# Optimization experiments

Measured on AMD Instinct MI355X. Metric: run time of the kernel, lower is better.

The kernel has to match this reference:

```python
import jax, jax.numpy as jnp
import numpy as np

NUM_HEADS = 16
HEAD_DIM = 64  # hidden_size // num_heads


def _logsparse_allowed(seq_len):
    # allowed[i, j] True if key j is attended by query i:
    # j == i, j == i-1, or j == i - 2^k (k >= 1); combined with causal (j <= i).
    i = jnp.arange(seq_len)[:, None]
    j = jnp.arange(seq_len)[None, :]
    diff = i - j
    pow2 = (diff > 0) & ((diff & (diff - 1)) == 0)  # covers diff==1 and diff==2^k
    return (diff == 0) | pow2  # implies diff >= 0, so causal is subsumed


def setup_inputs() -> dict:
    key = jax.random.key(0)
    ks = jax.random.split(key, 7)
    B, S, H = 4, 2048, 1024
    return {
        "hidden_states": jax.random.normal(ks[0], (B, S, H), dtype=jnp.float32),
        "attention_mask": jnp.zeros((B, 1, 1, S), dtype=jnp.float32),
        "Wq": jax.random.normal(ks[1], (H, H), dtype=jnp.float32) * 0.02,
        "bq": jnp.zeros((H,), dtype=jnp.float32),
        "Wk": jax.random.normal(ks[2], (H, H), dtype=jnp.float32) * 0.02,
        "bk": jnp.zeros((H,), dtype=jnp.float32),
        "Wv": jax.random.normal(ks[3], (H, H), dtype=jnp.float32) * 0.02,
        "bv": jnp.zeros((H,), dtype=jnp.float32),
    }


def _split_heads(x):
    B, S, _ = x.shape
    return x.reshape(B, S, NUM_HEADS, HEAD_DIM).transpose(0, 2, 1, 3)  # b h t d


def reference(hidden_states, attention_mask, Wq, bq, Wk, bk, Wv, bv):
    B, S, H = hidden_states.shape
    q = _split_heads(hidden_states @ Wq.T + bq)
    k = _split_heads(hidden_states @ Wk.T + bk)
    v = _split_heads(hidden_states @ Wv.T + bv)

    scores = jnp.einsum("bhqd,bhkd->bhqk", q, k) * (HEAD_DIM ** -0.5)
    allowed = _logsparse_allowed(S)  # [S, S] bool
    scores = jnp.where(allowed[None, None], scores, -jnp.inf)
    scores = scores + attention_mask  # [B,1,1,S] additive mask
    probs = jax.nn.softmax(scores, axis=-1)
    out = jnp.einsum("bhqk,bhkd->bhqd", probs, v)
    return out.transpose(0, 2, 1, 3).reshape(B, S, H)
```

## Files before the change

### kernel.cpp

```cpp
#include <hip/hip_runtime.h>
#include <hip/hip_bf16.h>

#define S_LEN   2048
#define NHEADS  16
#define HDIM    64
#define HID     1024
#define BATCH   4
#define M_ROWS  (BATCH * S_LEN)

#define BM 128
#define BN 128
#define BK 64

typedef __attribute__((ext_vector_type(8))) short short8;
typedef __attribute__((ext_vector_type(4))) float floatx4;
typedef __attribute__((ext_vector_type(16))) float floatx16;
typedef __attribute__((ext_vector_type(4))) unsigned short ushort4v;

__device__ __forceinline__ unsigned short f2bf_rne(float x) {
  union { float f; unsigned u; } v; v.f = x;
  unsigned r = v.u + 0x7fffu + ((v.u >> 16) & 1u);
  return (unsigned short)(r >> 16);
}

__device__ __forceinline__ float bf2f(unsigned short u) {
  union { unsigned u; float f; } c; c.u = ((unsigned)u) << 16;
  return c.f;
}

__device__ __forceinline__ void glds16(const unsigned short* g, unsigned short* l) {
  __builtin_amdgcn_global_load_lds(
      (const __attribute__((address_space(1))) unsigned int*)g,
      (__attribute__((address_space(3))) unsigned int*)l, 16, 0, 0);
}

#define HS4 (M_ROWS * HID / 4)
#define W4  (HID * HID / 4)
__global__ __launch_bounds__(256) void cast_all(
    const float* __restrict__ hs, const float* __restrict__ Wq,
    const float* __restrict__ Wk, const float* __restrict__ Wv,
    unsigned short* __restrict__ hsb, unsigned short* __restrict__ wqb,
    unsigned short* __restrict__ wkb, unsigned short* __restrict__ wvb) {
  int idx = blockIdx.x * 256 + threadIdx.x;
  const float* in;
  unsigned short* out;
  int off;
  if (idx < HS4) {
    in = hs; out = hsb; off = idx;
  } else {
    int r = idx - HS4;
    int seg = r >> 18;
    off = r & (W4 - 1);
    in  = (seg == 0) ? Wq  : (seg == 1) ? Wk  : Wv;
    out = (seg == 0) ? wqb : (seg == 1) ? wkb : wvb;
  }
  floatx4 v = __builtin_nontemporal_load((const floatx4*)in + off);
  ushort4v o;
  o.x = f2bf_rne(v.x);
  o.y = f2bf_rne(v.y);
  o.z = f2bf_rne(v.z);
  o.w = f2bf_rne(v.w);
  ((ushort4v*)out)[off] = o;
}

__global__ __launch_bounds__(256) void qkv_gemm(
    const unsigned short* __restrict__ A,
    const unsigned short* __restrict__ W0, const unsigned short* __restrict__ W1,
    const unsigned short* __restrict__ W2,
    const float* __restrict__ b0, const float* __restrict__ b1,
    const float* __restrict__ b2,
    unsigned short* __restrict__ O0, unsigned short* __restrict__ O1,
    unsigned short* __restrict__ O2) {
  const int K = HID;
  const int N = HID;
  const int z = blockIdx.z;
  const unsigned short* __restrict__ W = (z == 0) ? W0 : (z == 1) ? W1 : W2;
  const float* __restrict__ bias = (z == 0) ? b0 : (z == 1) ? b1 : b2;
  unsigned short* __restrict__ O = (z == 0) ? O0 : (z == 1) ? O1 : O2;

  __shared__ __align__(16) unsigned short As[BM * BK];
  __shared__ __align__(16) unsigned short Bs[BN * BK];

  const int tid = threadIdx.x;
  const int w = tid >> 6;
  const int lane = tid & 63;
  const int m0 = blockIdx.x * BM;
  const int n0 = blockIdx.y * BN;

  const int lr = lane >> 3;
  const int cc = (lane & 7) ^ lr;
  const unsigned short* gA[4];
  const unsigned short* gB[4];
  unsigned short* lA[4];
  unsigned short* lB[4];
  #pragma unroll
  for (int u = 0; u < 4; ++u) {
    const int seg = w * 4 + u;
    const int r = seg * 8 + lr;
    gA[u] = A + (size_t)(m0 + r) * K + cc * 8;
    gB[u] = W + (size_t)(n0 + r) * K + cc * 8;
    lA[u] = As + seg * 512;
    lB[u] = Bs + seg * 512;
  }

  const int lrow32 = lane & 31;
  const int kgrp = lane >> 5;
  const int sw = lane & 7;
  const int arow = (w & 1) * 64;
  const int brow = (w >> 1) * 64;

  floatx16 acc[2][2] = {};

  for (int k0 = 0; k0 < K; k0 += BK) {
    #pragma unroll
    for (int u = 0; u < 4; ++u) {
      glds16(gA[u] + k0, lA[u]);
      glds16(gB[u] + k0, lB[u]);
    }
    __syncthreads();

    #pragma unroll
    for (int s = 0; s < 4; ++s) {
      const int cp = (((s << 1) | kgrp) ^ sw) * 8;
      short8 af[2], bf[2];
      #pragma unroll
      for (int im = 0; im < 2; ++im)
        af[im] = *(const short8*)(As + (arow + im * 32 + lrow32) * BK + cp);
      #pragma unroll
      for (int in = 0; in < 2; ++in)
        bf[in] = *(const short8*)(Bs + (brow + in * 32 + lrow32) * BK + cp);

      #pragma unroll
      for (int im = 0; im < 2; ++im)
        #pragma unroll
        for (int in = 0; in < 2; ++in)
          acc[im][in] = __builtin_amdgcn_mfma_f32_32x32x16_bf16(af[im], bf[in], acc[im][in], 0, 0, 0);
    }
    __syncthreads();
  }

  #pragma unroll
  for (int im = 0; im < 2; ++im) {
    #pragma unroll
    for (int in = 0; in < 2; ++in) {
      const int col = n0 + brow + in * 32 + lrow32;
      const float bb = bias[col];
      const int rowbase = m0 + arow + im * 32 + 4 * kgrp;
      #pragma unroll
      for (int reg = 0; reg < 16; ++reg) {
        const int row = rowbase + (reg & 3) + 8 * (reg >> 2);
        O[(size_t)row * N + col] = f2bf_rne(acc[im][in][reg] + bb);
      }
    }
  }
}

__global__ __launch_bounds__(256) void logsparse_attn(
    const unsigned short* __restrict__ Q, const unsigned short* __restrict__ K,
    const unsigned short* __restrict__ V, const float* __restrict__ mask,
    float* __restrict__ out) {
  const int bid = (blockIdx.x & 7) * 512 + (blockIdx.x >> 3);
  const int tid = threadIdx.x;
  const int l = tid & 7;
  const int qglob = bid * 32 + (tid >> 3);

  const int i = qglob & (S_LEN - 1);
  const int h = (qglob >> 11) & (NHEADS - 1);
  const int b = qglob >> 15;

  const size_t base = (size_t)b * S_LEN * HID + h * HDIM + l * 8;

  int js[12];
  js[0] = i;
  int nj = 1;
  for (int d = 1; d <= i; d <<= 1) js[nj++] = i - d;
  #pragma unroll
  for (int t = 0; t < 12; ++t)
    if (t >= nj) js[t] = i;

  short8 k8[12];
  #pragma unroll
  for (int t = 0; t < 12; ++t)
    k8[t] = *(const short8*)(K + base + (size_t)js[t] * HID);
  const short8 q8 = *(const short8*)(Q + base + (size_t)i * HID);
  float mk[12];
  #pragma unroll
  for (int t = 0; t < 12; ++t)
    mk[t] = mask[b * S_LEN + js[t]];

  float qf[8];
  #pragma unroll
  for (int e = 0; e < 8; ++e) qf[e] = bf2f((unsigned short)q8[e]);

  float s[12];
  #pragma unroll
  for (int t = 0; t < 12; ++t) {
    float p = 0.f;
    #pragma unroll
    for (int e = 0; e < 8; ++e) p += qf[e] * bf2f((unsigned short)k8[t][e]);
    p += __shfl_xor(p, 1, 64);
    p += __shfl_xor(p, 2, 64);
    p += __shfl_xor(p, 4, 64);
    s[t] = (t < nj) ? (p * 0.125f + mk[t]) : -1e30f;
  }

  float mx = s[0];
  #pragma unroll
  for (int t = 1; t < 12; ++t) mx = fmaxf(mx, s[t]);
  float lsum = 0.f;
  #pragma unroll
  for (int t = 0; t < 12; ++t) { s[t] = __expf(s[t] - mx); lsum += s[t]; }
  const float inv = 1.f / lsum;

  short8 v8[12];
  #pragma unroll
  for (int t = 0; t < 12; ++t)
    v8[t] = *(const short8*)(V + base + (size_t)js[t] * HID);

  float o[8] = {};
  #pragma unroll
  for (int t = 0; t < 12; ++t) {
    #pragma unroll
    for (int e = 0; e < 8; ++e) o[e] += s[t] * bf2f((unsigned short)v8[t][e]);
  }

  float* op = out + base + (size_t)i * HID;
  floatx4 o0 = {o[0] * inv, o[1] * inv, o[2] * inv, o[3] * inv};
  floatx4 o1 = {o[4] * inv, o[5] * inv, o[6] * inv, o[7] * inv};
  __builtin_nontemporal_store(o0, (floatx4*)op);
  __builtin_nontemporal_store(o1, (floatx4*)(op + 4));
}

extern "C" void kernel_launch(void* const* d_in, const int* in_sizes, int n_in,
                              void* d_out, int out_size, void* d_ws, size_t ws_size,
                              hipStream_t stream) {
  const float* hs   = (const float*)d_in[0];
  const float* mask = (const float*)d_in[1];
  const float* Wq   = (const float*)d_in[2];
  const float* bq   = (const float*)d_in[3];
  const float* Wk   = (const float*)d_in[4];
  const float* bk   = (const float*)d_in[5];
  const float* Wv   = (const float*)d_in[6];
  const float* bv   = (const float*)d_in[7];
  float* out = (float*)d_out;

  unsigned short* hsb = (unsigned short*)d_ws;
  unsigned short* wqb = hsb + (size_t)M_ROWS * HID;
  unsigned short* wkb = wqb + (size_t)HID * HID;
  unsigned short* wvb = wkb + (size_t)HID * HID;
  unsigned short* Qb = wvb + (size_t)HID * HID;
  unsigned short* Kb = Qb + (size_t)M_ROWS * HID;
  unsigned short* Vb = Kb + (size_t)M_ROWS * HID;

  {
    int quads = HS4 + 3 * W4;
    cast_all<<<quads / 256, 256, 0, stream>>>(hs, Wq, Wk, Wv, hsb, wqb, wkb, wvb);
  }

  {
    dim3 grid(M_ROWS / BM, HID / BN, 3);
    qkv_gemm<<<grid, 256, 0, stream>>>(hsb, wqb, wkb, wvb, bq, bk, bv, Qb, Kb, Vb);
  }

  {
    int blocks = (BATCH * NHEADS * S_LEN) / 32;
    logsparse_attn<<<blocks, 256, 0, stream>>>(Qb, Kb, Vb, mask, out);
  }
}
```

Measured before the change: 181.1 us.

## Interleave K and V per head and retune GEMM LDS swizzle

The QKV GEMM now writes K and V into one interleaved buffer: each head's 64 K columns sit next to its 64 V columns in each 128-element row segment. The attention kernel uses 16 lanes per query, split into two halves that load K and V from the same row at once. The halves exchange dot products with a shuffle, and only the V half writes output. The LDS swizzle also XORs in the segment index to change the bank mapping. This aims to make the gathered K/V rows contiguous 256-byte reads and to cut per-thread register use, at the cost of twice as many threads and redundant softmax work in each half.

```diff
diff --git a/kernel.cpp b/kernel.cpp
--- a/kernel.cpp
+++ b/kernel.cpp
@@ -69,14 +69,11 @@
     const unsigned short* __restrict__ W2,
     const float* __restrict__ b0, const float* __restrict__ b1,
     const float* __restrict__ b2,
-    unsigned short* __restrict__ O0, unsigned short* __restrict__ O1,
-    unsigned short* __restrict__ O2) {
+    unsigned short* __restrict__ Qo, unsigned short* __restrict__ KVo) {
   const int K = HID;
-  const int N = HID;
   const int z = blockIdx.z;
   const unsigned short* __restrict__ W = (z == 0) ? W0 : (z == 1) ? W1 : W2;
   const float* __restrict__ bias = (z == 0) ? b0 : (z == 1) ? b1 : b2;
-  unsigned short* __restrict__ O = (z == 0) ? O0 : (z == 1) ? O1 : O2;
 
   __shared__ __align__(16) unsigned short As[BM * BK];
   __shared__ __align__(16) unsigned short Bs[BN * BK];
@@ -88,7 +85,6 @@
   const int n0 = blockIdx.y * BN;
 
   const int lr = lane >> 3;
-  const int cc = (lane & 7) ^ lr;
   const unsigned short* gA[4];
   const unsigned short* gB[4];
   unsigned short* lA[4];
@@ -96,6 +92,7 @@
   #pragma unroll
   for (int u = 0; u < 4; ++u) {
     const int seg = w * 4 + u;
+    const int cc = (lane & 7) ^ lr ^ (2 * (seg & 3));
     const int r = seg * 8 + lr;
     gA[u] = A + (size_t)(m0 + r) * K + cc * 8;
     gB[u] = W + (size_t)(n0 + r) * K + cc * 8;
@@ -105,7 +102,7 @@
 
   const int lrow32 = lane & 31;
   const int kgrp = lane >> 5;
-  const int sw = lane & 7;
+  const int sw = (lane & 7) ^ (2 * ((lane >> 3) & 3));
   const int arow = (w & 1) * 64;
   const int brow = (w >> 1) * 64;
 
@@ -139,36 +136,42 @@
     __syncthreads();
   }
 
+  unsigned short* const Ob = (z == 0) ? Qo : KVo;
+  const int ostride = (z == 0) ? HID : 2 * HID;
   #pragma unroll
   for (int im = 0; im < 2; ++im) {
     #pragma unroll
     for (int in = 0; in < 2; ++in) {
       const int col = n0 + brow + in * 32 + lrow32;
       const float bb = bias[col];
+      const int ocol = (z == 0) ? col
+                                : ((col >> 6) * 128 + (col & 63) + ((z == 2) ? 64 : 0));
       const int rowbase = m0 + arow + im * 32 + 4 * kgrp;
       #pragma unroll
       for (int reg = 0; reg < 16; ++reg) {
         const int row = rowbase + (reg & 3) + 8 * (reg >> 2);
-        O[(size_t)row * N + col] = f2bf_rne(acc[im][in][reg] + bb);
+        Ob[(size_t)row * ostride + ocol] = f2bf_rne(acc[im][in][reg] + bb);
       }
     }
   }
 }
 
 __global__ __launch_bounds__(256) void logsparse_attn(
-    const unsigned short* __restrict__ Q, const unsigned short* __restrict__ K,
-    const unsigned short* __restrict__ V, const float* __restrict__ mask,
-    float* __restrict__ out) {
-  const int bid = (blockIdx.x & 7) * 512 + (blockIdx.x >> 3);
+    const unsigned short* __restrict__ Q, const unsigned short* __restrict__ KV,
+    const float* __restrict__ mask, float* __restrict__ out) {
+  const int bid = (blockIdx.x & 7) * 1024 + (blockIdx.x >> 3);
   const int tid = threadIdx.x;
-  const int l = tid & 7;
-  const int qglob = bid * 32 + (tid >> 3);
+  const int l = tid & 15;
+  const int half = l >> 3;
+  const int e8 = (l & 7) * 8;
+  const int qglob = bid * 16 + (tid >> 4);
 
   const int i = qglob & (S_LEN - 1);
   const int h = (qglob >> 11) & (NHEADS - 1);
   const int b = qglob >> 15;
 
-  const size_t base = (size_t)b * S_LEN * HID + h * HDIM + l * 8;
+  const size_t qaddr  = ((size_t)b * S_LEN + i) * HID + h * HDIM + e8;
+  const size_t kvbase = (size_t)b * S_LEN * (2 * HID) + h * 128 + half * 64 + e8;
 
   int js[12];
   js[0] = i;
@@ -178,11 +181,11 @@
   for (int t = 0; t < 12; ++t)
     if (t >= nj) js[t] = i;
 
-  short8 k8[12];
+  short8 kv[12];
   #pragma unroll
   for (int t = 0; t < 12; ++t)
-    k8[t] = *(const short8*)(K + base + (size_t)js[t] * HID);
-  const short8 q8 = *(const short8*)(Q + base + (size_t)i * HID);
+    kv[t] = *(const short8*)(KV + kvbase + (size_t)js[t] * (2 * HID));
+  const short8 q8 = *(const short8*)(Q + qaddr);
   float mk[12];
   #pragma unroll
   for (int t = 0; t < 12; ++t)
@@ -197,11 +200,13 @@
   for (int t = 0; t < 12; ++t) {
     float p = 0.f;
     #pragma unroll
-    for (int e = 0; e < 8; ++e) p += qf[e] * bf2f((unsigned short)k8[t][e]);
+    for (int e = 0; e < 8; ++e) p += qf[e] * bf2f((unsigned short)kv[t][e]);
     p += __shfl_xor(p, 1, 64);
     p += __shfl_xor(p, 2, 64);
     p += __shfl_xor(p, 4, 64);
-    s[t] = (t < nj) ? (p * 0.125f + mk[t]) : -1e30f;
+    const float px = __shfl_xor(p, 8, 64);
+    const float sc = half ? px : p;
+    s[t] = (t < nj) ? (sc * 0.125f + mk[t]) : -1e30f;
   }
 
   float mx = s[0];
@@ -212,23 +217,20 @@
   for (int t = 0; t < 12; ++t) { s[t] = __expf(s[t] - mx); lsum += s[t]; }
   const float inv = 1.f / lsum;
 
-  short8 v8[12];
-  #pragma unroll
-  for (int t = 0; t < 12; ++t)
-    v8[t] = *(const short8*)(V + base + (size_t)js[t] * HID);
-
   float o[8] = {};
   #pragma unroll
   for (int t = 0; t < 12; ++t) {
     #pragma unroll
-    for (int e = 0; e < 8; ++e) o[e] += s[t] * bf2f((unsigned short)v8[t][e]);
-  }
-
-  float* op = out + base + (size_t)i * HID;
-  floatx4 o0 = {o[0] * inv, o[1] * inv, o[2] * inv, o[3] * inv};
-  floatx4 o1 = {o[4] * inv, o[5] * inv, o[6] * inv, o[7] * inv};
-  __builtin_nontemporal_store(o0, (floatx4*)op);
-  __builtin_nontemporal_store(o1, (floatx4*)(op + 4));
+    for (int e = 0; e < 8; ++e) o[e] += s[t] * bf2f((unsigned short)kv[t][e]);
+  }
+
+  if (half) {
+    float* op = out + ((size_t)b * S_LEN + i) * HID + h * HDIM + e8;
+    floatx4 o0 = {o[0] * inv, o[1] * inv, o[2] * inv, o[3] * inv};
+    floatx4 o1 = {o[4] * inv, o[5] * inv, o[6] * inv, o[7] * inv};
+    __builtin_nontemporal_store(o0, (floatx4*)op);
+    __builtin_nontemporal_store(o1, (floatx4*)(op + 4));
+  }
 }
 
 extern "C" void kernel_launch(void* const* d_in, const int* in_sizes, int n_in,
@@ -248,9 +250,8 @@
   unsigned short* wqb = hsb + (size_t)M_ROWS * HID;
   unsigned short* wkb = wqb + (size_t)HID * HID;
   unsigned short* wvb = wkb + (size_t)HID * HID;
-  unsigned short* Qb = wvb + (size_t)HID * HID;
-  unsigned short* Kb = Qb + (size_t)M_ROWS * HID;
-  unsigned short* Vb = Kb + (size_t)M_ROWS * HID;
+  unsigned short* Qb  = wvb + (size_t)HID * HID;
+  unsigned short* KVb = Qb + (size_t)M_ROWS * HID;
 
   {
     int quads = HS4 + 3 * W4;
@@ -259,11 +260,11 @@
 
   {
     dim3 grid(M_ROWS / BM, HID / BN, 3);
-    qkv_gemm<<<grid, 256, 0, stream>>>(hsb, wqb, wkb, wvb, bq, bk, bv, Qb, Kb, Vb);
+    qkv_gemm<<<grid, 256, 0, stream>>>(hsb, wqb, wkb, wvb, bq, bk, bv, Qb, KVb);
   }
 
   {
-    int blocks = (BATCH * NHEADS * S_LEN) / 32;
-    logsparse_attn<<<blocks, 256, 0, stream>>>(Qb, Kb, Vb, mask, out);
-  }
-}
+    int blocks = (BATCH * NHEADS * S_LEN) / 16;
+    logsparse_attn<<<blocks, 256, 0, stream>>>(Qb, KVb, mask, out);
+  }
+}
```

Measured after the change: 202.1 us. 1.12x slower.
